# Kernel optimization log

Measured on AMD Instinct MI355X. Metric: run time of the kernel, lower is better.

## Reference

```python
import jax, jax.numpy as jnp
import numpy as np

D_MODEL, N_HEAD, D_HEAD = 1024, 16, 64
QLEN, MLEN, BSZ = 1024, 512, 4
KLEN = QLEN + MLEN
RLEN = QLEN + KLEN
SCALE = 1.0 / (D_HEAD ** 0.5)
LN_EPS = 1e-12


def rel_shift(x, klen):
    # x: [i, j, b, n] -> shifted [i, klen, b, n]
    i, j, b, n = x.shape
    x = x.reshape(j, i, b, n)[1:].reshape(i, j - 1, b, n)
    return x[:, :klen]


def layer_norm(x, gamma, beta, eps=LN_EPS):
    mu = jnp.mean(x, axis=-1, keepdims=True)
    var = jnp.mean(jnp.square(x - mu), axis=-1, keepdims=True)
    return (x - mu) * jax.lax.rsqrt(var + eps) * gamma + beta


def setup_inputs() -> dict:
    key = jax.random.key(0)
    ks = jax.random.split(key, 16)
    std = 0.02
    h = jax.random.normal(ks[0], (QLEN, BSZ, D_MODEL), jnp.float32)
    r = jax.random.normal(ks[1], (RLEN, BSZ, D_MODEL), jnp.float32)
    mems = jax.random.normal(ks[2], (MLEN, BSZ, D_MODEL), jnp.float32)
    # binary float mask (1 = masked), broadcast over head dim
    attn_mask = (jax.random.uniform(ks[3], (QLEN, KLEN, BSZ, 1)) < 0.1).astype(jnp.float32)
    # one-hot segment matrix over 2 segment classes
    seg_ids = jax.random.randint(ks[4], (QLEN, KLEN, BSZ), 0, 2)
    seg_mat = jax.nn.one_hot(seg_ids, 2, dtype=jnp.float32)
    Wq = std * jax.random.normal(ks[5], (D_MODEL, N_HEAD, D_HEAD), jnp.float32)
    Wk = std * jax.random.normal(ks[6], (D_MODEL, N_HEAD, D_HEAD), jnp.float32)
    Wv = std * jax.random.normal(ks[7], (D_MODEL, N_HEAD, D_HEAD), jnp.float32)
    Wo = std * jax.random.normal(ks[8], (D_MODEL, N_HEAD, D_HEAD), jnp.float32)
    Wr = std * jax.random.normal(ks[9], (D_MODEL, N_HEAD, D_HEAD), jnp.float32)
    r_w_bias = jnp.zeros((N_HEAD, D_HEAD), jnp.float32)
    r_r_bias = jnp.zeros((N_HEAD, D_HEAD), jnp.float32)
    r_s_bias = jnp.zeros((N_HEAD, D_HEAD), jnp.float32)
    seg_embed = std * jax.random.normal(ks[10], (2, N_HEAD, D_HEAD), jnp.float32)
    ln_gamma = jnp.ones((D_MODEL,), jnp.float32)
    ln_beta = jnp.zeros((D_MODEL,), jnp.float32)
    return dict(h=h, r=r, mems=mems, attn_mask=attn_mask, seg_mat=seg_mat,
                Wq=Wq, Wk=Wk, Wv=Wv, Wo=Wo, Wr=Wr,
                r_w_bias=r_w_bias, r_r_bias=r_r_bias, r_s_bias=r_s_bias,
                seg_embed=seg_embed, ln_gamma=ln_gamma, ln_beta=ln_beta)


def reference(h, r, mems, attn_mask, seg_mat, Wq, Wk, Wv, Wo, Wr,
              r_w_bias, r_r_bias, r_s_bias, seg_embed, ln_gamma, ln_beta):
    cat = jnp.concatenate([mems, h], axis=0)  # [klen, b, d_model]
    q_head = jnp.einsum('ibh,hnd->ibnd', h, Wq)
    k_head_h = jnp.einsum('jbh,hnd->jbnd', cat, Wk)
    v_head_h = jnp.einsum('jbh,hnd->jbnd', cat, Wv)
    k_head_r = jnp.einsum('jbh,hnd->jbnd', r, Wr)

    klen = k_head_h.shape[0]
    ac = jnp.einsum('ibnd,jbnd->ijbn', q_head + r_w_bias, k_head_h)
    bd = jnp.einsum('ibnd,jbnd->ijbn', q_head + r_r_bias, k_head_r)
    bd = rel_shift(bd, klen)
    ef = jnp.einsum('ibnd,snd->ibns', q_head + r_s_bias, seg_embed)
    ef = jnp.einsum('ijbs,ibns->ijbn', seg_mat, ef)

    attn_score = (ac + bd + ef) * SCALE - 1e30 * attn_mask
    attn_prob = jax.nn.softmax(attn_score, axis=1)
    attn_vec = jnp.einsum('ijbn,jbnd->ibnd', attn_prob, v_head_h)

    attn_out = jnp.einsum('ibnd,hnd->ibh', attn_vec, Wo) + h  # residual
    return layer_norm(attn_out, ln_gamma, ln_beta)
```

## Files before the change

### kernel.cpp

```cpp
#include <hip/hip_runtime.h>

typedef unsigned short u16;
typedef __attribute__((ext_vector_type(8))) short bf16x8;
typedef __attribute__((ext_vector_type(4))) float f32x4;

constexpr int DM = 1024;
constexpr int NH = 16;
constexpr int DH = 64;
constexpr int QL = 1024;
constexpr int ML = 512;
constexpr int KL = 1536;
constexpr int RL = 2560;
constexpr int BS = 4;
constexpr int JT = KL / 64;
constexpr float SCALE = 0.125f;

static __device__ __forceinline__ u16 f2bf(float f) {
    unsigned u = __float_as_uint(f);
    u += 0x7fffu + ((u >> 16) & 1u);
    return (u16)(u >> 16);
}

static __device__ __forceinline__ void glds16(const u16* g, u16* l) {
    __builtin_amdgcn_global_load_lds(
        (const __attribute__((address_space(1))) unsigned int*)g,
        (__attribute__((address_space(3))) unsigned int*)l,
        16, 0, 0);
}

__global__ __launch_bounds__(256) void convert_kernel(
    const float* __restrict__ mems, const float* __restrict__ h,
    const float* __restrict__ r, const float* __restrict__ Wo,
    u16* __restrict__ catb, u16* __restrict__ rb, u16* __restrict__ wob)
{
    const long C0 = (long)ML * BS * DM;
    const long C1 = (long)KL * BS * DM;
    const long C2 = C1 + (long)RL * BS * DM;
    const long C3 = C2 + (long)DM * DM;
    long g = ((long)blockIdx.x * blockDim.x + threadIdx.x) * 4;
    if (g >= C3) return;
    const float* src; u16* dst;
    if (g < C0)      { src = mems + g;        dst = catb + g; }
    else if (g < C1) { src = h + (g - C0);    dst = catb + g; }
    else if (g < C2) { src = r + (g - C1);    dst = rb + (g - C1); }
    else             { src = Wo + (g - C2);   dst = wob + (g - C2); }
    float4 v = *(const float4*)src;
    unsigned lo = (unsigned)f2bf(v.x) | ((unsigned)f2bf(v.y) << 16);
    unsigned hi = (unsigned)f2bf(v.z) | ((unsigned)f2bf(v.w) << 16);
    *(uint2*)dst = make_uint2(lo, hi);
}

__global__ __launch_bounds__(256) void pack_kernel(
    const float* __restrict__ mask, const float* __restrict__ segm,
    ulonglong2* __restrict__ pk)
{
    __shared__ float mk[256];
    __shared__ float sg[256];
    const int i = blockIdx.x / JT;
    const int jt = blockIdx.x % JT;
    const int t = threadIdx.x;
    const size_t base = ((size_t)i * KL + jt * 64) * BS;
    mk[t] = mask[base + t];
    float2 s2 = ((const float2*)(segm + base * 2))[t];
    sg[t] = s2.y;
    __syncthreads();
    const int b = t >> 6, lane = t & 63;
    const unsigned long long mb = __ballot(mk[lane * 4 + b] > 0.5f);
    const unsigned long long sb = __ballot(sg[lane * 4 + b] > 0.5f);
    if (lane == 0) {
        ulonglong2 v; v.x = mb; v.y = sb;
        pk[((size_t)b * QL + i) * JT + jt] = v;
    }
}

__global__ __launch_bounds__(256) void transpose_w_kernel(
    const float* __restrict__ Wq, const float* __restrict__ Wk,
    const float* __restrict__ Wv, const float* __restrict__ Wr,
    u16* __restrict__ WqT, u16* __restrict__ WkT,
    u16* __restrict__ WvT, u16* __restrict__ WrT)
{
    __shared__ float tile[64][65];
    const float* W; u16* WT;
    switch (blockIdx.z) {
        case 0:  W = Wq; WT = WqT; break;
        case 1:  W = Wk; WT = WkT; break;
        case 2:  W = Wv; WT = WvT; break;
        default: W = Wr; WT = WrT; break;
    }
    const int k0 = blockIdx.x * 64, n0 = blockIdx.y * 64;
    const int tr = threadIdx.x >> 6, tc = threadIdx.x & 63;
    #pragma unroll
    for (int rr = 0; rr < 16; rr++) {
        int r = tr + rr * 4;
        tile[r][tc] = W[(size_t)(k0 + r) * DM + n0 + tc];
    }
    __syncthreads();
    #pragma unroll
    for (int rr = 0; rr < 16; rr++) {
        int n = tr + rr * 4;
        WT[(size_t)(n0 + n) * DM + k0 + tc] = f2bf(tile[tc][n]);
    }
}

__global__ __launch_bounds__(256) void proj_kernel(
    const u16* __restrict__ hb, const u16* __restrict__ catb,
    const u16* __restrict__ rb,
    const u16* __restrict__ WqT, const u16* __restrict__ WkT,
    const u16* __restrict__ WvT, const u16* __restrict__ WrT,
    float* __restrict__ q_s, u16* __restrict__ k_s,
    u16* __restrict__ v_s, u16* __restrict__ kr_s)
{
    __shared__ u16 a_lds[128][32];
    __shared__ u16 b_lds[128][32];
    const int id = blockIdx.x;
    const u16 *A, *B; void* C; int SEQ, MODE, local;
    if (id < 256)       { A = hb;   B = WqT; C = q_s;  SEQ = QL; MODE = 1; local = id; }
    else if (id < 640)  { A = catb; B = WkT; C = k_s;  SEQ = KL; MODE = 2; local = id - 256; }
    else if (id < 1024) { A = catb; B = WvT; C = v_s;  SEQ = KL; MODE = 2; local = id - 640; }
    else                { A = rb;   B = WrT; C = kr_s; SEQ = RL; MODE = 2; local = id - 1024; }
    const int bm = local >> 3, bnn = local & 7;

    const int t = threadIdx.x;
    const int w = t >> 6, lane = t & 63, l15 = lane & 15, q4 = lane >> 4;
    const int wm = (w >> 1) * 64, wn = (w & 1) * 64;
    const int srow = w * 32 + (lane >> 2);
    const int scol = (lane & 3) * 8;
    const u16* Ab = A + (size_t)(bm * 128 + srow) * DM + scol;
    const u16* Bb = B + (size_t)(bnn * 128 + srow) * DM + scol;
    u16* a_dst = &a_lds[w * 32][0];
    u16* b_dst = &b_lds[w * 32][0];

    f32x4 acc[4][4] = {};

    for (int k0 = 0; k0 < DM; k0 += 32) {
        __syncthreads();
        glds16(Ab + k0,           a_dst);
        glds16(Ab + k0 + 16 * DM, a_dst + 16 * 32);
        glds16(Bb + k0,           b_dst);
        glds16(Bb + k0 + 16 * DM, b_dst + 16 * 32);
        __syncthreads();
        bf16x8 af[4], bf[4];
        #pragma unroll
        for (int rt = 0; rt < 4; rt++)
            af[rt] = *(const bf16x8*)&a_lds[wm + rt * 16 + l15][q4 * 8];
        #pragma unroll
        for (int ct = 0; ct < 4; ct++)
            bf[ct] = *(const bf16x8*)&b_lds[wn + ct * 16 + l15][q4 * 8];
        #pragma unroll
        for (int rt = 0; rt < 4; rt++)
            #pragma unroll
            for (int ct = 0; ct < 4; ct++)
                acc[rt][ct] = __builtin_amdgcn_mfma_f32_16x16x32_bf16(
                    af[rt], bf[ct], acc[rt][ct], 0, 0, 0);
    }

    #pragma unroll
    for (int rt = 0; rt < 4; rt++)
      #pragma unroll
      for (int ct = 0; ct < 4; ct++)
        #pragma unroll
        for (int rg = 0; rg < 4; rg++) {
            const int R = bm * 128 + wm + rt * 16 + q4 * 4 + rg;
            const int Cc = bnn * 128 + wn + ct * 16 + l15;
            const float v = acc[rt][ct][rg];
            const int sq = R >> 2, bb = R & 3, hn = Cc >> 6, dd = Cc & 63;
            const size_t idx = ((size_t)(bb * NH + hn) * SEQ + sq) * DH + dd;
            if (MODE == 1) ((float*)C)[idx] = v;
            else           ((u16*)C)[idx]  = f2bf(v);
        }
}

__global__ __launch_bounds__(256) void vtrans_kernel(
    const u16* __restrict__ v_s, u16* __restrict__ vt_s)
{
    __shared__ u16 tl[64][72];
    const int j0 = blockIdx.x * 64;
    const int bn = blockIdx.y;
    const u16* vin = v_s + (size_t)bn * KL * DH;
    u16* vout = vt_s + (size_t)bn * DH * KL;
    const int t = threadIdx.x;
    const int r = t >> 3, c8 = (t & 7) * 8;
    #pragma unroll
    for (int it = 0; it < 64; it += 32)
        *(uint4*)&tl[r + it][c8] = *(const uint4*)(vin + (size_t)(j0 + r + it) * DH + c8);
    __syncthreads();
    #pragma unroll
    for (int it = 0; it < 64; it += 32) {
        const int d = r + it;
        u16 tmp[8];
        #pragma unroll
        for (int jj = 0; jj < 8; jj++) tmp[jj] = tl[c8 + jj][d];
        *(uint4*)&vout[(size_t)d * KL + j0 + c8] = *(const uint4*)tmp;
    }
}

__global__ __launch_bounds__(256) void ogemm_kernel(
    const u16* __restrict__ A, const u16* __restrict__ B,
    float* __restrict__ Cout)
{
    __shared__ u16 a_lds[128][32];
    __shared__ u16 b_lds[128][32];
    const int bm = blockIdx.x, bnn = blockIdx.y;
    const int t = threadIdx.x;
    const int w = t >> 6, lane = t & 63, l15 = lane & 15, q4 = lane >> 4;
    const int wm = (w >> 1) * 64, wn = (w & 1) * 64;
    const int srow = w * 32 + (lane >> 2);
    const int scol = (lane & 3) * 8;
    const u16* Ab = A + (size_t)(bm * 128 + srow) * DM + scol;
    const u16* Bb = B + (size_t)(bnn * 128 + srow) * DM + scol;
    u16* a_dst = &a_lds[w * 32][0];
    u16* b_dst = &b_lds[w * 32][0];

    f32x4 acc[4][4] = {};

    for (int k0 = 0; k0 < DM; k0 += 32) {
        __syncthreads();
        glds16(Ab + k0,           a_dst);
        glds16(Ab + k0 + 16 * DM, a_dst + 16 * 32);
        glds16(Bb + k0,           b_dst);
        glds16(Bb + k0 + 16 * DM, b_dst + 16 * 32);
        __syncthreads();
        bf16x8 af[4], bf[4];
        #pragma unroll
        for (int rt = 0; rt < 4; rt++)
            af[rt] = *(const bf16x8*)&a_lds[wm + rt * 16 + l15][q4 * 8];
        #pragma unroll
        for (int ct = 0; ct < 4; ct++)
            bf[ct] = *(const bf16x8*)&b_lds[wn + ct * 16 + l15][q4 * 8];
        #pragma unroll
        for (int rt = 0; rt < 4; rt++)
            #pragma unroll
            for (int ct = 0; ct < 4; ct++)
                acc[rt][ct] = __builtin_amdgcn_mfma_f32_16x16x32_bf16(
                    af[rt], bf[ct], acc[rt][ct], 0, 0, 0);
    }

    #pragma unroll
    for (int rt = 0; rt < 4; rt++)
      #pragma unroll
      for (int ct = 0; ct < 4; ct++)
        #pragma unroll
        for (int rg = 0; rg < 4; rg++) {
            const int R = bm * 128 + wm + rt * 16 + q4 * 4 + rg;
            const int C = bnn * 128 + wn + ct * 16 + l15;
            Cout[(size_t)R * DM + C] = acc[rt][ct][rg];
        }
}

__global__ __launch_bounds__(256, 3) void attn_kernel(
    const float* __restrict__ q_s, const u16* __restrict__ k_s,
    const u16* __restrict__ vt_s, const u16* __restrict__ kr_s,
    const ulonglong2* __restrict__ pk,
    const float* __restrict__ rwb, const float* __restrict__ rrb,
    const float* __restrict__ rsb, const float* __restrict__ seg_embed,
    u16* __restrict__ av_s)
{
    __shared__ u16 k2[2][64][32];
    __shared__ u16 vt2[2][64][32];
    __shared__ u16 p_lds[4][16][72];
    __shared__ float e_lds[2][64];

    const int itile = blockIdx.x;
    const int bn = blockIdx.y;
    const int b = bn >> 4, n = bn & 15;
    const int t = threadIdx.x;
    const int w = t >> 6, lane = t & 63, l15 = lane & 15, q4 = lane >> 4;
    const int i0 = itile * 64;
    const int ib = i0 + w * 16;

    const float* q_bn = q_s + (size_t)bn * QL * DH;
    const u16* k_bn   = k_s  + (size_t)bn * KL * DH;
    const u16* vt_bn  = vt_s + (size_t)bn * DH * KL;
    const u16* kr_bn  = kr_s + (size_t)bn * RL * DH;
    const ulonglong2* pk_b = pk + (size_t)b * QL * JT;

    if (t < 128) {
        const int rr = t >> 1, s = t & 1;
        const float* qrow = q_bn + (size_t)(i0 + rr) * DH;
        const float* se = seg_embed + (s * NH + n) * DH;
        const float* bias = rsb + n * DH;
        float acc = 0.f;
        #pragma unroll 16
        for (int d = 0; d < DH; d++) acc += (qrow[d] + bias[d]) * se[d];
        e_lds[s][rr] = acc;
    }

    bf16x8 qw[2], qr[2];
    {
        const float* qrow = q_bn + (size_t)(ib + l15) * DH;
        const float* bw = rwb + n * DH;
        const float* br = rrb + n * DH;
        #pragma unroll
        for (int kk = 0; kk < 2; kk++) {
            const int dbase = kk * 32 + q4 * 8;
            #pragma unroll
            for (int j = 0; j < 8; j++) {
                float qv = qrow[dbase + j];
                qw[kk][j] = (short)f2bf(qv + bw[dbase + j]);
                qr[kk][j] = (short)f2bf(qv + br[dbase + j]);
            }
        }
    }

    const int srow = lane >> 2;
    const int sseg = (lane & 3) * 8;
    const u16* kg = k_bn  + (size_t)(w * 16 + srow) * DH + sseg;
    const u16* vg = vt_bn + (size_t)(w * 16 + srow) * KL + sseg;
    u16* kd0 = &k2[0][w * 16][0];
    u16* kd1 = &k2[1][w * 16][0];
    u16* vd0 = &vt2[0][w * 16][0];
    u16* vd1 = &vt2[1][w * 16][0];

    f32x4 o[4] = {};
    float l_r[4] = {0.f, 0.f, 0.f, 0.f};

    bf16x8 krv[10];
    {
        const int p0 = QL - ib - 15;
        #pragma unroll
        for (int wc = 0; wc < 5; wc++) {
            const u16* kp = kr_bn + (size_t)(p0 + wc * 16 + l15) * DH + q4 * 8;
            krv[wc * 2]     = *(const bf16x8*)kp;
            krv[wc * 2 + 1] = *(const bf16x8*)(kp + 32);
        }
    }

    for (int jt = 0; jt < JT; jt++) {
        const int j0 = jt * 64;
        __syncthreads();
        glds16(kg + (size_t)j0 * DH,      kd0);
        glds16(kg + (size_t)j0 * DH + 32, kd1);
        glds16(vg + j0,                   vd0);
        glds16(vg + j0 + 32,              vd1);
        ulonglong2 mp[4];
        #pragma unroll
        for (int rg = 0; rg < 4; rg++)
            mp[rg] = pk_b[(size_t)(ib + q4 * 4 + rg) * JT + jt];
        __syncthreads();

        f32x4 sac[4] = {};
        #pragma unroll
        for (int ct = 0; ct < 4; ct++) {
            bf16x8 kb0 = *(const bf16x8*)&k2[0][ct * 16 + l15][q4 * 8];
            bf16x8 kb1 = *(const bf16x8*)&k2[1][ct * 16 + l15][q4 * 8];
            sac[ct] = __builtin_amdgcn_mfma_f32_16x16x32_bf16(qw[0], kb0, sac[ct], 0, 0, 0);
            sac[ct] = __builtin_amdgcn_mfma_f32_16x16x32_bf16(qw[1], kb1, sac[ct], 0, 0, 0);
        }

        f32x4 bacc[5] = {};
        #pragma unroll
        for (int wc = 0; wc < 5; wc++) {
            bacc[wc] = __builtin_amdgcn_mfma_f32_16x16x32_bf16(qr[0], krv[wc * 2],     bacc[wc], 0, 0, 0);
            bacc[wc] = __builtin_amdgcn_mfma_f32_16x16x32_bf16(qr[1], krv[wc * 2 + 1], bacc[wc], 0, 0, 0);
        }

        if (jt + 1 < JT) {
            const int p0n = j0 + 64 + QL - ib - 15;
            #pragma unroll
            for (int wc = 0; wc < 5; wc++) {
                const u16* kp = kr_bn + (size_t)(p0n + wc * 16 + l15) * DH + q4 * 8;
                krv[wc * 2]     = *(const bf16x8*)kp;
                krv[wc * 2 + 1] = *(const bf16x8*)(kp + 32);
            }
        }

        #pragma unroll
        for (int rg = 0; rg < 4; rg++) {
            const int row = q4 * 4 + rg;
            const int v = l15 + 15 - row;
            const int srcl = (q4 << 4) | (v & 15);
            float sh[5];
            #pragma unroll
            for (int w5 = 0; w5 < 5; w5++)
                sh[w5] = __shfl(bacc[w5][rg], srcl, 64);
            const float e0 = e_lds[0][w * 16 + row];
            const float e1 = e_lds[1][w * 16 + row];
            float s0 = 0.f;
            #pragma unroll
            for (int ct = 0; ct < 4; ct++) {
                const float bd = (v < 16) ? sh[ct] : sh[ct + 1];
                const int bit = ct * 16 + l15;
                const float ef = ((mp[rg].y >> bit) & 1ull) ? e1 : e0;
                float s = (sac[ct][rg] + bd + ef) * SCALE;
                s = ((mp[rg].x >> bit) & 1ull) ? -1e30f : s;
                const float p = __expf(s);
                p_lds[w][row][ct * 16 + l15] = f2bf(p);
                s0 += p;
            }
            #pragma unroll
            for (int off = 1; off < 16; off <<= 1)
                s0 += __shfl_xor(s0, off, 64);
            l_r[rg] += s0;
        }

        #pragma unroll
        for (int kk = 0; kk < 2; kk++) {
            bf16x8 pf = *(const bf16x8*)&p_lds[w][l15][kk * 32 + q4 * 8];
            #pragma unroll
            for (int dt = 0; dt < 4; dt++) {
                bf16x8 vf = *(const bf16x8*)&vt2[kk][dt * 16 + l15][q4 * 8];
                o[dt] = __builtin_amdgcn_mfma_f32_16x16x32_bf16(pf, vf, o[dt], 0, 0, 0);
            }
        }
    }

    #pragma unroll
    for (int dt = 0; dt < 4; dt++)
        #pragma unroll
        for (int rg = 0; rg < 4; rg++) {
            const int row = q4 * 4 + rg;
            const int ii = ib + row;
            const int d = dt * 16 + l15;
            const float v = o[dt][rg] / l_r[rg];
            av_s[(size_t)(ii * BS + b) * DM + n * DH + d] = f2bf(v);
        }
}

__global__ __launch_bounds__(256) void ln_kernel(
    const float* __restrict__ ao, const float* __restrict__ h,
    const float* __restrict__ gamma, const float* __restrict__ beta,
    float* __restrict__ out)
{
    __shared__ float red[8];
    const int row = blockIdx.x, t = threadIdx.x;
    const float* a  = ao + (size_t)row * DM;
    const float* hh = h  + (size_t)row * DM;
    float4 av = *(const float4*)(a + t * 4);
    float4 hv = *(const float4*)(hh + t * 4);
    const float x0 = av.x + hv.x, x1 = av.y + hv.y;
    const float x2 = av.z + hv.z, x3 = av.w + hv.w;
    float s = x0 + x1 + x2 + x3;
    float s2 = x0 * x0 + x1 * x1 + x2 * x2 + x3 * x3;
    #pragma unroll
    for (int off = 1; off < 64; off <<= 1) {
        s  += __shfl_xor(s, off, 64);
        s2 += __shfl_xor(s2, off, 64);
    }
    const int w = t >> 6;
    if ((t & 63) == 0) { red[w] = s; red[4 + w] = s2; }
    __syncthreads();
    s  = red[0] + red[1] + red[2] + red[3];
    s2 = red[4] + red[5] + red[6] + red[7];
    const float mu = s * (1.f / DM);
    const float var = s2 * (1.f / DM) - mu * mu;
    const float rstd = rsqrtf(var + 1e-12f);
    float4 g  = *(const float4*)(gamma + t * 4);
    float4 bb = *(const float4*)(beta + t * 4);
    float4 ov;
    ov.x = (x0 - mu) * rstd * g.x + bb.x;
    ov.y = (x1 - mu) * rstd * g.y + bb.y;
    ov.z = (x2 - mu) * rstd * g.z + bb.z;
    ov.w = (x3 - mu) * rstd * g.w + bb.w;
    *(float4*)(out + (size_t)row * DM + t * 4) = ov;
}

extern "C" void kernel_launch(void* const* d_in, const int* in_sizes, int n_in,
                              void* d_out, int out_size, void* d_ws, size_t ws_size,
                              hipStream_t stream) {
    (void)in_sizes; (void)n_in; (void)out_size; (void)ws_size;
    const float* h    = (const float*)d_in[0];
    const float* r    = (const float*)d_in[1];
    const float* mems = (const float*)d_in[2];
    const float* mask = (const float*)d_in[3];
    const float* segm = (const float*)d_in[4];
    const float* Wq   = (const float*)d_in[5];
    const float* Wk   = (const float*)d_in[6];
    const float* Wv   = (const float*)d_in[7];
    const float* Wo   = (const float*)d_in[8];
    const float* Wr   = (const float*)d_in[9];
    const float* rwb  = (const float*)d_in[10];
    const float* rrb  = (const float*)d_in[11];
    const float* rsb  = (const float*)d_in[12];
    const float* semb = (const float*)d_in[13];
    const float* gam  = (const float*)d_in[14];
    const float* bet  = (const float*)d_in[15];
    float* out = (float*)d_out;

    char* wsb = (char*)d_ws;
    size_t off = 0;
    auto alloc = [&](size_t bytes) -> void* {
        void* p = wsb + off; off += (bytes + 255) & ~(size_t)255; return p;
    };
    u16* catb = (u16*)alloc((size_t)KL * BS * DM * 2);
    u16* rb   = (u16*)alloc((size_t)RL * BS * DM * 2);
    u16* WqT  = (u16*)alloc((size_t)DM * DM * 2);
    u16* WkT  = (u16*)alloc((size_t)DM * DM * 2);
    u16* WvT  = (u16*)alloc((size_t)DM * DM * 2);
    u16* WrT  = (u16*)alloc((size_t)DM * DM * 2);
    u16* WoB  = (u16*)alloc((size_t)DM * DM * 2);
    float* q_s = (float*)alloc((size_t)BS * NH * QL * DH * 4);
    u16* k_s  = (u16*)alloc((size_t)BS * NH * KL * DH * 2);
    u16* vt_s = (u16*)alloc((size_t)BS * NH * KL * DH * 2);
    u16* kr_s = (u16*)alloc((size_t)BS * NH * RL * DH * 2 + 8192);
    u16* av_s = (u16*)alloc((size_t)QL * BS * DM * 2);
    float* ao_s = (float*)alloc((size_t)QL * BS * DM * 4);
    ulonglong2* pk = (ulonglong2*)alloc((size_t)BS * QL * JT * 16);
    u16* v_s = (u16*)ao_s;

    convert_kernel<<<17408, 256, 0, stream>>>(mems, h, r, Wo, catb, rb, WoB);
    pack_kernel<<<QL * JT, 256, 0, stream>>>(mask, segm, pk);
    transpose_w_kernel<<<dim3(16, 16, 4), 256, 0, stream>>>(Wq, Wk, Wv, Wr, WqT, WkT, WvT, WrT);
    const u16* hb = catb + (size_t)2048 * DM;
    proj_kernel<<<1664, 256, 0, stream>>>(hb, catb, rb, WqT, WkT, WvT, WrT,
                                          q_s, k_s, v_s, kr_s);
    vtrans_kernel<<<dim3(JT, 64), 256, 0, stream>>>(v_s, vt_s);
    attn_kernel<<<dim3(16, 64), 256, 0, stream>>>(q_s, k_s, vt_s, kr_s, pk,
                                                  rwb, rrb, rsb, semb, av_s);
    ogemm_kernel<<<dim3(32, 8), 256, 0, stream>>>(av_s, WoB, ao_s);
    ln_kernel<<<4096, 256, 0, stream>>>(ao_s, h, gam, bet, out);
}
```

Baseline: 590.6 us.

## Merge prep kernels and stage relative-key tiles through swizzled LDS

Three preprocessing kernels (convert, mask/segment pack, weight transpose) are merged into one launch that dispatches on block index, removing two launch gaps. In the attention kernel, the per-wave register prefetch of relative-position key rows is replaced by a block-wide asynchronous global-to-LDS load of a 128-row window with XOR swizzling. The 16-row overlaps between waves are now loaded once per block instead of separately by each wave. This adds 16KB of LDS per block, which may lower occupancy against the 3-blocks launch bound, and drops the register double-buffering of the next tile.

```diff
diff --git a/kernel.cpp b/kernel.cpp
--- a/kernel.cpp
+++ b/kernel.cpp
@@ -28,77 +28,79 @@
         16, 0, 0);
 }
 
-__global__ __launch_bounds__(256) void convert_kernel(
+__global__ __launch_bounds__(256) void prep_kernel(
     const float* __restrict__ mems, const float* __restrict__ h,
     const float* __restrict__ r, const float* __restrict__ Wo,
-    u16* __restrict__ catb, u16* __restrict__ rb, u16* __restrict__ wob)
-{
-    const long C0 = (long)ML * BS * DM;
-    const long C1 = (long)KL * BS * DM;
-    const long C2 = C1 + (long)RL * BS * DM;
-    const long C3 = C2 + (long)DM * DM;
-    long g = ((long)blockIdx.x * blockDim.x + threadIdx.x) * 4;
-    if (g >= C3) return;
-    const float* src; u16* dst;
-    if (g < C0)      { src = mems + g;        dst = catb + g; }
-    else if (g < C1) { src = h + (g - C0);    dst = catb + g; }
-    else if (g < C2) { src = r + (g - C1);    dst = rb + (g - C1); }
-    else             { src = Wo + (g - C2);   dst = wob + (g - C2); }
-    float4 v = *(const float4*)src;
-    unsigned lo = (unsigned)f2bf(v.x) | ((unsigned)f2bf(v.y) << 16);
-    unsigned hi = (unsigned)f2bf(v.z) | ((unsigned)f2bf(v.w) << 16);
-    *(uint2*)dst = make_uint2(lo, hi);
-}
-
-__global__ __launch_bounds__(256) void pack_kernel(
     const float* __restrict__ mask, const float* __restrict__ segm,
+    const float* __restrict__ Wq, const float* __restrict__ Wk,
+    const float* __restrict__ Wv, const float* __restrict__ Wr,
+    u16* __restrict__ catb, u16* __restrict__ rb, u16* __restrict__ wob,
+    u16* __restrict__ WqT, u16* __restrict__ WkT,
+    u16* __restrict__ WvT, u16* __restrict__ WrT,
     ulonglong2* __restrict__ pk)
 {
-    __shared__ float mk[256];
-    __shared__ float sg[256];
-    const int i = blockIdx.x / JT;
-    const int jt = blockIdx.x % JT;
+    __shared__ float smem[64 * 65];
+    const int id = blockIdx.x;
     const int t = threadIdx.x;
-    const size_t base = ((size_t)i * KL + jt * 64) * BS;
-    mk[t] = mask[base + t];
-    float2 s2 = ((const float2*)(segm + base * 2))[t];
-    sg[t] = s2.y;
-    __syncthreads();
-    const int b = t >> 6, lane = t & 63;
-    const unsigned long long mb = __ballot(mk[lane * 4 + b] > 0.5f);
-    const unsigned long long sb = __ballot(sg[lane * 4 + b] > 0.5f);
-    if (lane == 0) {
-        ulonglong2 v; v.x = mb; v.y = sb;
-        pk[((size_t)b * QL + i) * JT + jt] = v;
-    }
-}
-
-__global__ __launch_bounds__(256) void transpose_w_kernel(
-    const float* __restrict__ Wq, const float* __restrict__ Wk,
-    const float* __restrict__ Wv, const float* __restrict__ Wr,
-    u16* __restrict__ WqT, u16* __restrict__ WkT,
-    u16* __restrict__ WvT, u16* __restrict__ WrT)
-{
-    __shared__ float tile[64][65];
-    const float* W; u16* WT;
-    switch (blockIdx.z) {
-        case 0:  W = Wq; WT = WqT; break;
-        case 1:  W = Wk; WT = WkT; break;
-        case 2:  W = Wv; WT = WvT; break;
-        default: W = Wr; WT = WrT; break;
-    }
-    const int k0 = blockIdx.x * 64, n0 = blockIdx.y * 64;
-    const int tr = threadIdx.x >> 6, tc = threadIdx.x & 63;
-    #pragma unroll
-    for (int rr = 0; rr < 16; rr++) {
-        int r = tr + rr * 4;
-        tile[r][tc] = W[(size_t)(k0 + r) * DM + n0 + tc];
-    }
-    __syncthreads();
-    #pragma unroll
-    for (int rr = 0; rr < 16; rr++) {
-        int n = tr + rr * 4;
-        WT[(size_t)(n0 + n) * DM + k0 + tc] = f2bf(tile[tc][n]);
+
+    if (id < 17408) {
+        const long C0 = (long)ML * BS * DM;
+        const long C1 = (long)KL * BS * DM;
+        const long C2 = C1 + (long)RL * BS * DM;
+        long g = ((long)id * 256 + t) * 4;
+        const float* src; u16* dst;
+        if (g < C0)      { src = mems + g;        dst = catb + g; }
+        else if (g < C1) { src = h + (g - C0);    dst = catb + g; }
+        else if (g < C2) { src = r + (g - C1);    dst = rb + (g - C1); }
+        else             { src = Wo + (g - C2);   dst = wob + (g - C2); }
+        float4 v = *(const float4*)src;
+        unsigned lo = (unsigned)f2bf(v.x) | ((unsigned)f2bf(v.y) << 16);
+        unsigned hi = (unsigned)f2bf(v.z) | ((unsigned)f2bf(v.w) << 16);
+        *(uint2*)dst = make_uint2(lo, hi);
+        return;
+    }
+    if (id < 18432) {
+        float (*tile)[65] = (float(*)[65])smem;
+        const int local = id - 17408;
+        const float* W; u16* WT;
+        switch (local >> 8) {
+            case 0:  W = Wq; WT = WqT; break;
+            case 1:  W = Wk; WT = WkT; break;
+            case 2:  W = Wv; WT = WvT; break;
+            default: W = Wr; WT = WrT; break;
+        }
+        const int k0 = (local & 15) * 64, n0 = ((local >> 4) & 15) * 64;
+        const int tr = t >> 6, tc = t & 63;
+        #pragma unroll
+        for (int rr = 0; rr < 16; rr++) {
+            int rw = tr + rr * 4;
+            tile[rw][tc] = W[(size_t)(k0 + rw) * DM + n0 + tc];
+        }
+        __syncthreads();
+        #pragma unroll
+        for (int rr = 0; rr < 16; rr++) {
+            int n = tr + rr * 4;
+            WT[(size_t)(n0 + n) * DM + k0 + tc] = f2bf(tile[tc][n]);
+        }
+        return;
+    }
+    {
+        float* mk = smem;
+        float* sg = smem + 256;
+        const int local = id - 18432;
+        const int i = local / JT, jt = local - i * JT;
+        const size_t base = ((size_t)i * KL + jt * 64) * BS;
+        mk[t] = mask[base + t];
+        float2 s2 = ((const float2*)(segm + base * 2))[t];
+        sg[t] = s2.y;
+        __syncthreads();
+        const int b = t >> 6, lane = t & 63;
+        const unsigned long long mb = __ballot(mk[lane * 4 + b] > 0.5f);
+        const unsigned long long sb = __ballot(sg[lane * 4 + b] > 0.5f);
+        if (lane == 0) {
+            ulonglong2 v; v.x = mb; v.y = sb;
+            pk[((size_t)b * QL + i) * JT + jt] = v;
+        }
     }
 }
 
@@ -257,6 +259,7 @@
 {
     __shared__ u16 k2[2][64][32];
     __shared__ u16 vt2[2][64][32];
+    __shared__ u16 krl[128][64];
     __shared__ u16 p_lds[4][16][72];
     __shared__ float e_lds[2][64];
 
@@ -311,27 +314,31 @@
     u16* vd0 = &vt2[0][w * 16][0];
     u16* vd1 = &vt2[1][w * 16][0];
 
+    const int krow = lane >> 3;
+    const int ksrcseg = (lane & 7) ^ krow;
+    u16* krd = &krl[w * 32][0];
+
     f32x4 o[4] = {};
     float l_r[4] = {0.f, 0.f, 0.f, 0.f};
 
-    bf16x8 krv[10];
-    {
-        const int p0 = QL - ib - 15;
-        #pragma unroll
-        for (int wc = 0; wc < 5; wc++) {
-            const u16* kp = kr_bn + (size_t)(p0 + wc * 16 + l15) * DH + q4 * 8;
-            krv[wc * 2]     = *(const bf16x8*)kp;
-            krv[wc * 2 + 1] = *(const bf16x8*)(kp + 32);
-        }
-    }
+    const int lrb = 48 - w * 16 + l15;
+    const int sA = ((q4)     ^ (l15 & 7)) * 8;
+    const int sB = ((q4 + 4) ^ (l15 & 7)) * 8;
 
     for (int jt = 0; jt < JT; jt++) {
         const int j0 = jt * 64;
+        const int Pbase = j0 + QL - i0 - 63;
         __syncthreads();
         glds16(kg + (size_t)j0 * DH,      kd0);
         glds16(kg + (size_t)j0 * DH + 32, kd1);
         glds16(vg + j0,                   vd0);
         glds16(vg + j0 + 32,              vd1);
+        {
+            const u16* krg = kr_bn + (size_t)(Pbase + w * 32 + krow) * DH + ksrcseg * 8;
+            #pragma unroll
+            for (int m = 0; m < 4; m++)
+                glds16(krg + (size_t)m * 8 * DH, krd + m * 8 * 64);
+        }
         ulonglong2 mp[4];
         #pragma unroll
         for (int rg = 0; rg < 4; rg++)
@@ -350,18 +357,10 @@
         f32x4 bacc[5] = {};
         #pragma unroll
         for (int wc = 0; wc < 5; wc++) {
-            bacc[wc] = __builtin_amdgcn_mfma_f32_16x16x32_bf16(qr[0], krv[wc * 2],     bacc[wc], 0, 0, 0);
-            bacc[wc] = __builtin_amdgcn_mfma_f32_16x16x32_bf16(qr[1], krv[wc * 2 + 1], bacc[wc], 0, 0, 0);
-        }
-
-        if (jt + 1 < JT) {
-            const int p0n = j0 + 64 + QL - ib - 15;
-            #pragma unroll
-            for (int wc = 0; wc < 5; wc++) {
-                const u16* kp = kr_bn + (size_t)(p0n + wc * 16 + l15) * DH + q4 * 8;
-                krv[wc * 2]     = *(const bf16x8*)kp;
-                krv[wc * 2 + 1] = *(const bf16x8*)(kp + 32);
-            }
+            bf16x8 b0 = *(const bf16x8*)&krl[lrb + wc * 16][sA];
+            bf16x8 b1 = *(const bf16x8*)&krl[lrb + wc * 16][sB];
+            bacc[wc] = __builtin_amdgcn_mfma_f32_16x16x32_bf16(qr[0], b0, bacc[wc], 0, 0, 0);
+            bacc[wc] = __builtin_amdgcn_mfma_f32_16x16x32_bf16(qr[1], b1, bacc[wc], 0, 0, 0);
         }
 
         #pragma unroll
@@ -497,9 +496,10 @@
     ulonglong2* pk = (ulonglong2*)alloc((size_t)BS * QL * JT * 16);
     u16* v_s = (u16*)ao_s;
 
-    convert_kernel<<<17408, 256, 0, stream>>>(mems, h, r, Wo, catb, rb, WoB);
-    pack_kernel<<<QL * JT, 256, 0, stream>>>(mask, segm, pk);
-    transpose_w_kernel<<<dim3(16, 16, 4), 256, 0, stream>>>(Wq, Wk, Wv, Wr, WqT, WkT, WvT, WrT);
+    prep_kernel<<<43008, 256, 0, stream>>>(mems, h, r, Wo, mask, segm,
+                                           Wq, Wk, Wv, Wr,
+                                           catb, rb, WoB,
+                                           WqT, WkT, WvT, WrT, pk);
     const u16* hb = catb + (size_t)2048 * DM;
     proj_kernel<<<1664, 256, 0, stream>>>(hb, catb, rb, WqT, WkT, WvT, WrT,
                                           q_s, k_s, v_s, kr_s);
```

Result: faster. 530.3 us (-10.2%).
